# Kernel tuning notes

Hardware: AMD Instinct MI355X
Metric: run time of the kernel (lower is better)

## Reference

```python
import jax, jax.numpy as jnp
import numpy as np
import math

HEAD_DIM = 64

def setup_inputs() -> dict:
    key = jax.random.key(0)
    kq, kk, kv = jax.random.split(key, 3)
    B, H, S, D = 2, 16, 2048, HEAD_DIM
    Q = jax.random.normal(kq, (B, H, S, D), dtype=jnp.float32)
    K = jax.random.normal(kk, (B, H, S, D), dtype=jnp.float32)
    V = jax.random.normal(kv, (B, H, S, D), dtype=jnp.float32)
    mask = jnp.ones((B, S), dtype=jnp.float32)
    return {"Q": Q, "K": K, "V": V, "mask": mask}

def reference(Q, K, V, mask):
    # dot: [B, H, S, S]
    dot = jnp.einsum('bhqd,bhkd->bhqk', Q, K) / math.sqrt(HEAD_DIM)
    # additive mask: -1e6 where mask == 0 (mask broadcast over heads and query dim)
    dot = dot - 1000000.0 * (1.0 - mask[:, None, None, :])
    attn = jax.nn.softmax(dot, axis=-1)
    # dropout_prob = 0 -> identity
    X = jnp.einsum('bhqk,bhkd->bhqd', attn, V)
    return X
```

## Files before the change

### kernel.cpp

```cpp
#include <hip/hip_runtime.h>
#include <hip/hip_fp16.h>
#include <stdint.h>


#define S_LEN   2048
#define DHEAD   64
#define NPER    16
#define CEXP    9.0f
#define SCL2E   0.18033688011112042f
#define L2E     1.4426950408889634f

typedef __attribute__((ext_vector_type(4))) float    f32x4;
typedef __attribute__((ext_vector_type(2))) _Float16 f16x2;
typedef __attribute__((ext_vector_type(4))) _Float16 f16x4;
typedef __attribute__((ext_vector_type(8))) _Float16 f16x8;
typedef __attribute__((ext_vector_type(2))) __fp16   hf16x2;

static __device__ __forceinline__ float exp2_fast(float x) {
#if __has_builtin(__builtin_amdgcn_exp2f)
  return __builtin_amdgcn_exp2f(x);
#else
  float r;
  asm("v_exp_f32 %0, %1" : "=v"(r) : "v"(x));
  return r;
#endif
}

static __device__ __forceinline__ hf16x2 pkh(float a, float b) {
  return __builtin_amdgcn_cvt_pkrtz(a, b);
}
static __device__ __forceinline__ f16x2 h2f(hf16x2 h) {
  union { hf16x2 i; f16x2 o; } u; u.i = h; return u.o;
}

#define GLDS16(g, l)                                                  \
  __builtin_amdgcn_global_load_lds(                                   \
      (const __attribute__((address_space(1))) void*)(g),             \
      (__attribute__((address_space(3))) void*)(l), 16, 0, 0)

__global__ __launch_bounds__(256) void prep(
    const float* __restrict__ K, const float* __restrict__ V,
    const float* __restrict__ Mk, _Float16* __restrict__ Kswz,
    _Float16* __restrict__ Vg, float* __restrict__ madd_g) {
  const int gb = blockIdx.x;
  if (gb < 2048) {
    const int idx = gb * 256 + threadIdx.x;
    const int c  = idx & 7;
    const int kv = (idx >> 3) & 2047;
    const int bh = idx >> 14;
    const float* src = K + ((size_t)bh * S_LEN + kv) * DHEAD + c * 8;
    float4 a = *(const float4*)(src);
    float4 d = *(const float4*)(src + 4);
    union { f16x2 h[4]; f16x8 v; } r;
    r.h[0] = h2f(pkh(a.x, a.y)); r.h[1] = h2f(pkh(a.z, a.w));
    r.h[2] = h2f(pkh(d.x, d.y)); r.h[3] = h2f(pkh(d.z, d.w));
    *(f16x8*)(Kswz + ((size_t)bh * S_LEN + kv) * DHEAD + ((c + kv) & 7) * 8) = r.v;
    if (idx < 2 * S_LEN)
      madd_g[idx] = -CEXP - (1.0e6f * L2E) * (1.0f - Mk[idx]);
  } else {
    const int idx = (gb - 2048) * 256 + threadIdx.x;
    const int d  = idx & 63;
    const int g  = (idx >> 6) & 15;
    const int j  = (idx >> 10) & 31;
    const int bh = idx >> 15;
    const float* src = V + ((size_t)bh * S_LEN + j * 64 + g * 4) * DHEAD + d;
    float v0 = src[0], v1 = src[64], v2 = src[128], v3 = src[192];
    union { f16x2 h[2]; f16x4 v; } r;
    r.h[0] = h2f(pkh(v0, v1)); r.h[1] = h2f(pkh(v2, v3));
    *(f16x4*)(Vg + (size_t)idx * 4) = r.v;
  }
}

__global__ __launch_bounds__(256, 2) void attn_ws(
    const float* __restrict__ Q, const _Float16* __restrict__ Kswz,
    const _Float16* __restrict__ Vg, const float* __restrict__ madd_g,
    float* __restrict__ O) {
  __shared__ __align__(16) _Float16 kls[2][2][4096];
  __shared__ __align__(16) _Float16 vls[2][2][4096];
  __shared__ __align__(16) float    mls[2][2][64];

  const int tid  = threadIdx.x;
  const int lane = tid & 63;
  const int wave = tid >> 6;
  const int quad = lane >> 4;
  const int x    = lane & 15;

  const int blk  = blockIdx.x;
  const int bh   = (blk & 7) | (((blk >> 3) & 3) << 3);
  const int qblk = blk >> 5;
  const int b    = bh >> 4;

  const size_t base = (size_t)bh * S_LEN * DHEAD;
  const float*    Qb = Q + base;
  const _Float16* Kb = Kswz + base;
  const _Float16* Vb = Vg + base;
  const float*    Mb = madd_g + b * S_LEN;
  float* Ob = O + base;

  const int q0 = qblk * 128 + wave * 16 + x;
  f16x8 qf[2][2];
#pragma unroll
  for (int u = 0; u < 2; ++u) {
    const float* qp = Qb + (size_t)(q0 + u * 64) * DHEAD + quad * 8;
#pragma unroll
    for (int kb = 0; kb < 2; ++kb) {
      float4 a = *(const float4*)(qp + kb * 32);
      float4 c = *(const float4*)(qp + kb * 32 + 4);
      union { f16x2 h[4]; f16x8 v; } r;
      r.h[0] = h2f(pkh(a.x * SCL2E, a.y * SCL2E));
      r.h[1] = h2f(pkh(a.z * SCL2E, a.w * SCL2E));
      r.h[2] = h2f(pkh(c.x * SCL2E, c.y * SCL2E));
      r.h[3] = h2f(pkh(c.z * SCL2E, c.w * SCL2E));
      qf[u][kb] = r.v;
    }
  }

  auto prefetch = [&](int p, int bi) {
    const _Float16* ks = Kb + p * 8192 + tid * 8;
    const _Float16* vs = Vb + p * 8192 + tid * 8;
    _Float16* kd = &kls[bi][0][tid * 8];
    _Float16* vd = &vls[bi][0][tid * 8];
    GLDS16(ks,        kd);
    GLDS16(ks + 2048, kd + 2048);
    GLDS16(ks + 4096, kd + 4096);
    GLDS16(ks + 6144, kd + 6144);
    GLDS16(vs,        vd);
    GLDS16(vs + 2048, vd + 2048);
    GLDS16(vs + 4096, vd + 4096);
    GLDS16(vs + 6144, vd + 6144);
    if (tid < 32)
      GLDS16(Mb + p * 128 + tid * 4, &mls[bi][0][tid * 4]);
  };

  f32x4 xacc[2][4];
#pragma unroll
  for (int u = 0; u < 2; ++u)
#pragma unroll
    for (int m = 0; m < 4; ++m) xacc[u][m] = (f32x4){0.f, 0.f, 0.f, 0.f};
  float lsum[2] = {0.0f, 0.0f};
  const hf16x2 one2 = {(__fp16)1.0f, (__fp16)1.0f};

  prefetch(0, 0);
  __syncthreads();

  for (int p = 0; p < NPER; ++p) {
    const int cur = p & 1;
    if (p + 1 < NPER) prefetch(p + 1, cur ^ 1);

#pragma unroll
    for (int sub = 0; sub < 2; ++sub) {
      const _Float16* k0 = &kls[cur][sub][x * 64 + ((quad + x) & 7) * 8];
      const _Float16* k1 = &kls[cur][sub][x * 64 + ((quad + 4 + x) & 7) * 8];
      const float*    mp = &mls[cur][sub][quad * 4];
      f16x4 pf[2][4];
#pragma unroll
      for (int t = 0; t < 4; ++t) {
        f16x8 ka0 = *(const f16x8*)(k0 + t * 1024);
        f16x8 ka1 = *(const f16x8*)(k1 + t * 1024);
        f32x4 mi = *(const f32x4*)(mp + t * 16);
#pragma unroll
        for (int u = 0; u < 2; ++u) {
          f32x4 st = __builtin_amdgcn_mfma_f32_16x16x32_f16(ka0, qf[u][0], mi, 0, 0, 0);
          st = __builtin_amdgcn_mfma_f32_16x16x32_f16(ka1, qf[u][1], st, 0, 0, 0);
          hf16x2 h0 = pkh(exp2_fast(st.x), exp2_fast(st.y));
          hf16x2 h1 = pkh(exp2_fast(st.z), exp2_fast(st.w));
#if __has_builtin(__builtin_amdgcn_fdot2)
          lsum[u] = __builtin_amdgcn_fdot2(h0, one2, lsum[u], false);
          lsum[u] = __builtin_amdgcn_fdot2(h1, one2, lsum[u], false);
#else
          f16x2 a0 = h2f(h0), a1 = h2f(h1);
          lsum[u] += (float)a0.x + (float)a0.y + (float)a1.x + (float)a1.y;
#endif
          union { f16x2 h[2]; f16x4 v; } r;
          r.h[0] = h2f(h0);
          r.h[1] = h2f(h1);
          pf[u][t] = r.v;
        }
      }
      const _Float16* vbase = &vls[cur][sub][256 * quad + 4 * x];
#pragma unroll
      for (int m = 0; m < 4; ++m) {
        f32x4 x0 = xacc[0][m];
        f32x4 x1 = xacc[1][m];
#pragma unroll
        for (int t = 0; t < 4; ++t) {
          f16x4 vf = *(const f16x4*)(vbase + 1024 * t + 64 * m);
          x0 = __builtin_amdgcn_mfma_f32_16x16x16f16(vf, pf[0][t], x0, 0, 0, 0);
          x1 = __builtin_amdgcn_mfma_f32_16x16x16f16(vf, pf[1][t], x1, 0, 0, 0);
        }
        xacc[0][m] = x0;
        xacc[1][m] = x1;
      }
    }
    __syncthreads();
  }

#pragma unroll
  for (int u = 0; u < 2; ++u) {
    float l = lsum[u];
    l += __shfl_xor(l, 16, 64);
    l += __shfl_xor(l, 32, 64);
    const float rl = 1.0f / l;
    float* op = Ob + (size_t)(q0 + u * 64) * DHEAD;
#pragma unroll
    for (int m = 0; m < 4; ++m) {
      float4 o;
      o.x = xacc[u][m].x * rl; o.y = xacc[u][m].y * rl;
      o.z = xacc[u][m].z * rl; o.w = xacc[u][m].w * rl;
      *(float4*)(op + m * 16 + quad * 4) = o;
    }
  }
}

extern "C" void kernel_launch(void* const* d_in, const int* in_sizes, int n_in,
                              void* d_out, int out_size, void* d_ws, size_t ws_size,
                              hipStream_t stream) {
  const float* Q = (const float*)d_in[0];
  const float* K = (const float*)d_in[1];
  const float* V = (const float*)d_in[2];
  const float* M = (const float*)d_in[3];
  float* O = (float*)d_out;

  _Float16* Kswz = (_Float16*)d_ws;
  _Float16* Vg   = Kswz + 4194304;
  float*    madd = (float*)((char*)d_ws + 16777216);
  hipLaunchKernelGGL(prep, dim3(6144), dim3(256), 0, stream, K, V, M, Kswz, Vg, madd);
  hipLaunchKernelGGL(attn_ws, dim3(512), dim3(256), 0, stream, Q, Kswz, Vg, madd, O);
}
```

Baseline: 136.9 us.

## Use 512-thread blocks with one query tile per wave instead of two

Doubles the block to 8 waves. Each wave now handles 16 query rows instead of 32, which halves per-thread accumulator, Q-fragment and score registers so the launch bound can ask for 4 blocks per CU. The K/V tile prefetch is split over twice as many threads, so each issues half as many global-to-LDS loads. The trade is that each K/V tile read from LDS is shared across more waves, so more LDS reads and barrier cost per unit of MFMA work. The q0 indexing still uses wave*16 with 8 waves, so it covers 128 rows and stays consistent.

```diff
diff --git a/kernel.cpp b/kernel.cpp
--- a/kernel.cpp
+++ b/kernel.cpp
@@ -71,7 +71,7 @@
   }
 }
 
-__global__ __launch_bounds__(256, 2) void attn_ws(
+__global__ __launch_bounds__(512, 4) void attn_ws(
     const float* __restrict__ Q, const _Float16* __restrict__ Kswz,
     const _Float16* __restrict__ Vg, const float* __restrict__ madd_g,
     float* __restrict__ O) {
@@ -98,10 +98,9 @@
   float* Ob = O + base;
 
   const int q0 = qblk * 128 + wave * 16 + x;
-  f16x8 qf[2][2];
-#pragma unroll
-  for (int u = 0; u < 2; ++u) {
-    const float* qp = Qb + (size_t)(q0 + u * 64) * DHEAD + quad * 8;
+  f16x8 qf[2];
+  {
+    const float* qp = Qb + (size_t)q0 * DHEAD + quad * 8;
 #pragma unroll
     for (int kb = 0; kb < 2; ++kb) {
       float4 a = *(const float4*)(qp + kb * 32);
@@ -111,7 +110,7 @@
       r.h[1] = h2f(pkh(a.z * SCL2E, a.w * SCL2E));
       r.h[2] = h2f(pkh(c.x * SCL2E, c.y * SCL2E));
       r.h[3] = h2f(pkh(c.z * SCL2E, c.w * SCL2E));
-      qf[u][kb] = r.v;
+      qf[kb] = r.v;
     }
   }
 
@@ -121,23 +120,17 @@
     _Float16* kd = &kls[bi][0][tid * 8];
     _Float16* vd = &vls[bi][0][tid * 8];
     GLDS16(ks,        kd);
-    GLDS16(ks + 2048, kd + 2048);
     GLDS16(ks + 4096, kd + 4096);
-    GLDS16(ks + 6144, kd + 6144);
     GLDS16(vs,        vd);
-    GLDS16(vs + 2048, vd + 2048);
     GLDS16(vs + 4096, vd + 4096);
-    GLDS16(vs + 6144, vd + 6144);
     if (tid < 32)
       GLDS16(Mb + p * 128 + tid * 4, &mls[bi][0][tid * 4]);
   };
 
-  f32x4 xacc[2][4];
-#pragma unroll
-  for (int u = 0; u < 2; ++u)
-#pragma unroll
-    for (int m = 0; m < 4; ++m) xacc[u][m] = (f32x4){0.f, 0.f, 0.f, 0.f};
-  float lsum[2] = {0.0f, 0.0f};
+  f32x4 xacc[4];
+#pragma unroll
+  for (int m = 0; m < 4; ++m) xacc[m] = (f32x4){0.f, 0.f, 0.f, 0.f};
+  float lsum = 0.0f;
   const hf16x2 one2 = {(__fp16)1.0f, (__fp16)1.0f};
 
   prefetch(0, 0);
@@ -152,61 +145,54 @@
       const _Float16* k0 = &kls[cur][sub][x * 64 + ((quad + x) & 7) * 8];
       const _Float16* k1 = &kls[cur][sub][x * 64 + ((quad + 4 + x) & 7) * 8];
       const float*    mp = &mls[cur][sub][quad * 4];
-      f16x4 pf[2][4];
+      f16x4 pf[4];
 #pragma unroll
       for (int t = 0; t < 4; ++t) {
         f16x8 ka0 = *(const f16x8*)(k0 + t * 1024);
         f16x8 ka1 = *(const f16x8*)(k1 + t * 1024);
         f32x4 mi = *(const f32x4*)(mp + t * 16);
-#pragma unroll
-        for (int u = 0; u < 2; ++u) {
-          f32x4 st = __builtin_amdgcn_mfma_f32_16x16x32_f16(ka0, qf[u][0], mi, 0, 0, 0);
-          st = __builtin_amdgcn_mfma_f32_16x16x32_f16(ka1, qf[u][1], st, 0, 0, 0);
-          hf16x2 h0 = pkh(exp2_fast(st.x), exp2_fast(st.y));
-          hf16x2 h1 = pkh(exp2_fast(st.z), exp2_fast(st.w));
+        f32x4 st = __builtin_amdgcn_mfma_f32_16x16x32_f16(ka0, qf[0], mi, 0, 0, 0);
+        st = __builtin_amdgcn_mfma_f32_16x16x32_f16(ka1, qf[1], st, 0, 0, 0);
+        hf16x2 h0 = pkh(exp2_fast(st.x), exp2_fast(st.y));
+        hf16x2 h1 = pkh(exp2_fast(st.z), exp2_fast(st.w));
 #if __has_builtin(__builtin_amdgcn_fdot2)
-          lsum[u] = __builtin_amdgcn_fdot2(h0, one2, lsum[u], false);
-          lsum[u] = __builtin_amdgcn_fdot2(h1, one2, lsum[u], false);
+        lsum = __builtin_amdgcn_fdot2(h0, one2, lsum, false);
+        lsum = __builtin_amdgcn_fdot2(h1, one2, lsum, false);
 #else
-          f16x2 a0 = h2f(h0), a1 = h2f(h1);
-          lsum[u] += (float)a0.x + (float)a0.y + (float)a1.x + (float)a1.y;
+        f16x2 a0 = h2f(h0), a1 = h2f(h1);
+        lsum += (float)a0.x + (float)a0.y + (float)a1.x + (float)a1.y;
 #endif
-          union { f16x2 h[2]; f16x4 v; } r;
-          r.h[0] = h2f(h0);
-          r.h[1] = h2f(h1);
-          pf[u][t] = r.v;
-        }
+        union { f16x2 h[2]; f16x4 v; } r;
+        r.h[0] = h2f(h0);
+        r.h[1] = h2f(h1);
+        pf[t] = r.v;
       }
       const _Float16* vbase = &vls[cur][sub][256 * quad + 4 * x];
 #pragma unroll
       for (int m = 0; m < 4; ++m) {
-        f32x4 x0 = xacc[0][m];
-        f32x4 x1 = xacc[1][m];
+        f32x4 x0 = xacc[m];
 #pragma unroll
         for (int t = 0; t < 4; ++t) {
           f16x4 vf = *(const f16x4*)(vbase + 1024 * t + 64 * m);
-          x0 = __builtin_amdgcn_mfma_f32_16x16x16f16(vf, pf[0][t], x0, 0, 0, 0);
-          x1 = __builtin_amdgcn_mfma_f32_16x16x16f16(vf, pf[1][t], x1, 0, 0, 0);
+          x0 = __builtin_amdgcn_mfma_f32_16x16x16f16(vf, pf[t], x0, 0, 0, 0);
         }
-        xacc[0][m] = x0;
-        xacc[1][m] = x1;
+        xacc[m] = x0;
       }
     }
     __syncthreads();
   }
 
-#pragma unroll
-  for (int u = 0; u < 2; ++u) {
-    float l = lsum[u];
+  {
+    float l = lsum;
     l += __shfl_xor(l, 16, 64);
     l += __shfl_xor(l, 32, 64);
     const float rl = 1.0f / l;
-    float* op = Ob + (size_t)(q0 + u * 64) * DHEAD;
+    float* op = Ob + (size_t)q0 * DHEAD;
 #pragma unroll
     for (int m = 0; m < 4; ++m) {
       float4 o;
-      o.x = xacc[u][m].x * rl; o.y = xacc[u][m].y * rl;
-      o.z = xacc[u][m].z * rl; o.w = xacc[u][m].w * rl;
+      o.x = xacc[m].x * rl; o.y = xacc[m].y * rl;
+      o.z = xacc[m].z * rl; o.w = xacc[m].w * rl;
       *(float4*)(op + m * 16 + quad * 4) = o;
     }
   }
@@ -225,5 +211,5 @@
   _Float16* Vg   = Kswz + 4194304;
   float*    madd = (float*)((char*)d_ws + 16777216);
   hipLaunchKernelGGL(prep, dim3(6144), dim3(256), 0, stream, K, V, M, Kswz, Vg, madd);
-  hipLaunchKernelGGL(attn_ws, dim3(512), dim3(256), 0, stream, Q, Kswz, Vg, madd, O);
-}
+  hipLaunchKernelGGL(attn_ws, dim3(512), dim3(512), 0, stream, Q, Kswz, Vg, madd, O);
+}
```

Result: no change. 138.8 us (+1.3%).

## Load V fragments directly from global into registers, halve K tile size

Applied to the files above, without the earlier changes.

V fragments are no longer staged through LDS; each lane reads its V fragments straight from global memory into registers at the top of each iteration, so only K and mask tiles go through shared memory. The K/mask tile is halved to 64 keys per iteration, doubling the iteration count and the number of barriers. This cuts LDS traffic and footprint, which could allow higher occupancy. In exchange, every wave in the block reissues the same V reads, relying on cache hits, and global-load latency now sits in the critical path before the PV MFMAs.

```diff
diff --git a/kernel.cpp b/kernel.cpp
--- a/kernel.cpp
+++ b/kernel.cpp
@@ -5,7 +5,7 @@
 
 #define S_LEN   2048
 #define DHEAD   64
-#define NPER    16
+#define NTILE   32
 #define CEXP    9.0f
 #define SCL2E   0.18033688011112042f
 #define L2E     1.4426950408889634f
@@ -75,9 +75,7 @@
     const float* __restrict__ Q, const _Float16* __restrict__ Kswz,
     const _Float16* __restrict__ Vg, const float* __restrict__ madd_g,
     float* __restrict__ O) {
-  __shared__ __align__(16) _Float16 kls[2][2][4096];
-  __shared__ __align__(16) _Float16 vls[2][2][4096];
-  __shared__ __align__(16) float    mls[2][2][64];
+  __shared__ __align__(16) _Float16 smem[28672];
 
   const int tid  = threadIdx.x;
   const int lane = tid & 63;
@@ -96,6 +94,8 @@
   const _Float16* Vb = Vg + base;
   const float*    Mb = madd_g + b * S_LEN;
   float* Ob = O + base;
+
+  float* const mbase = (float*)(smem + 8192);
 
   const int q0 = qblk * 128 + wave * 16 + x;
   f16x8 qf[2][2];
@@ -116,21 +116,15 @@
   }
 
   auto prefetch = [&](int p, int bi) {
-    const _Float16* ks = Kb + p * 8192 + tid * 8;
-    const _Float16* vs = Vb + p * 8192 + tid * 8;
-    _Float16* kd = &kls[bi][0][tid * 8];
-    _Float16* vd = &vls[bi][0][tid * 8];
+    const _Float16* ks = Kb + (size_t)p * 4096 + tid * 8;
+    _Float16* kd = smem + bi * 4096 + tid * 8;
     GLDS16(ks,        kd);
     GLDS16(ks + 2048, kd + 2048);
-    GLDS16(ks + 4096, kd + 4096);
-    GLDS16(ks + 6144, kd + 6144);
-    GLDS16(vs,        vd);
-    GLDS16(vs + 2048, vd + 2048);
-    GLDS16(vs + 4096, vd + 4096);
-    GLDS16(vs + 6144, vd + 6144);
-    if (tid < 32)
-      GLDS16(Mb + p * 128 + tid * 4, &mls[bi][0][tid * 4]);
+    if (tid < 16)
+      GLDS16(Mb + p * 64 + tid * 4, mbase + bi * 64 + tid * 4);
   };
+
+  const _Float16* vlane = Vb + 256 * quad + 4 * x;
 
   f32x4 xacc[2][4];
 #pragma unroll
@@ -143,54 +137,59 @@
   prefetch(0, 0);
   __syncthreads();
 
-  for (int p = 0; p < NPER; ++p) {
+  for (int p = 0; p < NTILE; ++p) {
     const int cur = p & 1;
-    if (p + 1 < NPER) prefetch(p + 1, cur ^ 1);
-
-#pragma unroll
-    for (int sub = 0; sub < 2; ++sub) {
-      const _Float16* k0 = &kls[cur][sub][x * 64 + ((quad + x) & 7) * 8];
-      const _Float16* k1 = &kls[cur][sub][x * 64 + ((quad + 4 + x) & 7) * 8];
-      const float*    mp = &mls[cur][sub][quad * 4];
-      f16x4 pf[2][4];
+
+    const _Float16* vp = vlane + (size_t)p * 4096;
+    f16x4 vf[4][4];
+#pragma unroll
+    for (int t = 0; t < 4; ++t)
+#pragma unroll
+      for (int m = 0; m < 4; ++m)
+        vf[t][m] = *(const f16x4*)(vp + t * 1024 + m * 64);
+    __builtin_amdgcn_sched_barrier(0);
+
+    if (p + 1 < NTILE) prefetch(p + 1, cur ^ 1);
+
+    const _Float16* k0 = smem + cur * 4096 + x * 64 + ((quad + x) & 7) * 8;
+    const _Float16* k1 = smem + cur * 4096 + x * 64 + ((quad + 4 + x) & 7) * 8;
+    const float*    mp = mbase + cur * 64 + quad * 4;
+    f16x4 pf[2][4];
+#pragma unroll
+    for (int t = 0; t < 4; ++t) {
+      f16x8 ka0 = *(const f16x8*)(k0 + t * 1024);
+      f16x8 ka1 = *(const f16x8*)(k1 + t * 1024);
+      f32x4 mi = *(const f32x4*)(mp + t * 16);
+#pragma unroll
+      for (int u = 0; u < 2; ++u) {
+        f32x4 st = __builtin_amdgcn_mfma_f32_16x16x32_f16(ka0, qf[u][0], mi, 0, 0, 0);
+        st = __builtin_amdgcn_mfma_f32_16x16x32_f16(ka1, qf[u][1], st, 0, 0, 0);
+        hf16x2 h0 = pkh(exp2_fast(st.x), exp2_fast(st.y));
+        hf16x2 h1 = pkh(exp2_fast(st.z), exp2_fast(st.w));
+#if __has_builtin(__builtin_amdgcn_fdot2)
+        lsum[u] = __builtin_amdgcn_fdot2(h0, one2, lsum[u], false);
+        lsum[u] = __builtin_amdgcn_fdot2(h1, one2, lsum[u], false);
+#else
+        f16x2 a0 = h2f(h0), a1 = h2f(h1);
+        lsum[u] += (float)a0.x + (float)a0.y + (float)a1.x + (float)a1.y;
+#endif
+        union { f16x2 h[2]; f16x4 v; } r;
+        r.h[0] = h2f(h0);
+        r.h[1] = h2f(h1);
+        pf[u][t] = r.v;
+      }
+    }
+#pragma unroll
+    for (int m = 0; m < 4; ++m) {
+      f32x4 x0 = xacc[0][m];
+      f32x4 x1 = xacc[1][m];
 #pragma unroll
       for (int t = 0; t < 4; ++t) {
-        f16x8 ka0 = *(const f16x8*)(k0 + t * 1024);
-        f16x8 ka1 = *(const f16x8*)(k1 + t * 1024);
-        f32x4 mi = *(const f32x4*)(mp + t * 16);
-#pragma unroll
-        for (int u = 0; u < 2; ++u) {
-          f32x4 st = __builtin_amdgcn_mfma_f32_16x16x32_f16(ka0, qf[u][0], mi, 0, 0, 0);
-          st = __builtin_amdgcn_mfma_f32_16x16x32_f16(ka1, qf[u][1], st, 0, 0, 0);
-          hf16x2 h0 = pkh(exp2_fast(st.x), exp2_fast(st.y));
-          hf16x2 h1 = pkh(exp2_fast(st.z), exp2_fast(st.w));
-#if __has_builtin(__builtin_amdgcn_fdot2)
-          lsum[u] = __builtin_amdgcn_fdot2(h0, one2, lsum[u], false);
-          lsum[u] = __builtin_amdgcn_fdot2(h1, one2, lsum[u], false);
-#else
-          f16x2 a0 = h2f(h0), a1 = h2f(h1);
-          lsum[u] += (float)a0.x + (float)a0.y + (float)a1.x + (float)a1.y;
-#endif
-          union { f16x2 h[2]; f16x4 v; } r;
-          r.h[0] = h2f(h0);
-          r.h[1] = h2f(h1);
-          pf[u][t] = r.v;
-        }
+        x0 = __builtin_amdgcn_mfma_f32_16x16x16f16(vf[t][m], pf[0][t], x0, 0, 0, 0);
+        x1 = __builtin_amdgcn_mfma_f32_16x16x16f16(vf[t][m], pf[1][t], x1, 0, 0, 0);
       }
-      const _Float16* vbase = &vls[cur][sub][256 * quad + 4 * x];
-#pragma unroll
-      for (int m = 0; m < 4; ++m) {
-        f32x4 x0 = xacc[0][m];
-        f32x4 x1 = xacc[1][m];
-#pragma unroll
-        for (int t = 0; t < 4; ++t) {
-          f16x4 vf = *(const f16x4*)(vbase + 1024 * t + 64 * m);
-          x0 = __builtin_amdgcn_mfma_f32_16x16x16f16(vf, pf[0][t], x0, 0, 0, 0);
-          x1 = __builtin_amdgcn_mfma_f32_16x16x16f16(vf, pf[1][t], x1, 0, 0, 0);
-        }
-        xacc[0][m] = x0;
-        xacc[1][m] = x1;
-      }
+      xacc[0][m] = x0;
+      xacc[1][m] = x1;
     }
     __syncthreads();
   }
```

Result: slower. 142.3 us (+3.9%).
